# Kernel tuning notes

Measured on AMD Instinct MI355X. Metric: run time of the kernel, lower is better.

The kernel has to match this reference:

```python
import jax, jax.numpy as jnp
import numpy as np
from jax import lax

K = 5          # kernel_size
P = K // 2     # padding
DN = ('NCHW', 'OIHW', 'NCHW')


def _dwconv(z, wt, bt):
    # depthwise conv: z [b,c,h,w], wt [c,1,K,K], bt [c]
    c = z.shape[1]
    y = lax.conv_general_dilated(z, wt, (1, 1), [(P, P), (P, P)],
                                 feature_group_count=c, dimension_numbers=DN)
    return y + bt[None, :, None, None]


def setup_inputs() -> dict:
    key = jax.random.key(0)
    ks = jax.random.split(key, 8)
    b, c, h, w = 8, 64, 256, 256
    return {
        'x': jax.random.normal(ks[0], (b, c, h, w), jnp.float32),
        'w1': jax.random.normal(ks[1], (3, c, 1, K, K), jnp.float32) * 0.1,
        'b1': jax.random.normal(ks[2], (3, c), jnp.float32) * 0.1,
        'w2': jax.random.normal(ks[3], (3, c, 1, K, K), jnp.float32) * 0.1,
        'b2': jax.random.normal(ks[4], (3, c), jnp.float32) * 0.1,
        'wk': jax.random.normal(ks[5], (K * K * c, c), jnp.float32) * 0.1,
        'bk': jax.random.normal(ks[6], (K * K * c,), jnp.float32) * 0.1,
        'bias': jnp.zeros((c,), jnp.float32),
    }


def reference(x, w1, b1, w2, b2, wk, bk, bias):
    b, c, h, w = x.shape
    # avgpool 2x2 stride 2
    t = x.reshape(b, c, h // 2, 2, w // 2, 2).mean(axis=(3, 5))
    # Block1: 3 depthwise convs
    for i in range(3):
        t = _dwconv(t, w1[i], b1[i])
    # maxpool 2x2 stride 2
    hh, ww = t.shape[2], t.shape[3]
    t = t.reshape(b, c, hh // 2, 2, ww // 2, 2).max(axis=(3, 5))
    # Block2: 3 depthwise convs
    for i in range(3):
        t = _dwconv(t, w2[i], b2[i])
    # adaptive avg pool to 1x1 -> [b, c]
    g = t.mean(axis=(2, 3))
    # tokernel 1x1 conv -> per-sample depthwise kernels [b*c, 1, K, K]
    kern = (jnp.einsum('bc,oc->bo', g, wk) + bk).reshape(b * c, 1, K, K)
    # per-sample dynamic depthwise conv (groups = b*c)
    y = lax.conv_general_dilated(x.reshape(1, b * c, h, w), kern, (1, 1),
                                 [(P, P), (P, P)], feature_group_count=b * c,
                                 dimension_numbers=DN)
    return y.reshape(b, c, h, w) + bias[None, :, None, None]
```

## Files before the change

### kernel.cpp

```cpp
#include <hip/hip_runtime.h>

#define BB 8
#define CC 64
#define HH 256
#define WW 256
#define H1 128
#define W1 128
#define KK 5

template<int SS>
__device__ __forceinline__ void conv4x4(const float* __restrict__ src,
                                        const float* __restrict__ wr,
                                        float bv, float a[4][4])
{
#pragma unroll
    for (int i = 0; i < 4; i++)
#pragma unroll
        for (int j = 0; j < 4; j++) a[i][j] = bv;
#pragma unroll
    for (int ir = 0; ir < 8; ir++) {
        const float* s = src + ir * SS;
        float4 L = *(const float4*)s;
        float4 R = *(const float4*)(s + 4);
        float e[8] = {L.x, L.y, L.z, L.w, R.x, R.y, R.z, R.w};
#pragma unroll
        for (int i = 0; i < 4; i++) {
            const int ky = ir - i;
            if (ky >= 0 && ky < 5) {
#pragma unroll
                for (int kx = 0; kx < 5; kx++) {
                    const float wv = wr[ky * 5 + kx];
#pragma unroll
                    for (int j = 0; j < 4; j++) a[i][j] += e[j + kx] * wv;
                }
            }
        }
    }
}

template<int SS>
__device__ __forceinline__ void conv1x4(const float* __restrict__ src,
                                        const float* __restrict__ wr,
                                        float bv, float a[4])
{
#pragma unroll
    for (int j = 0; j < 4; j++) a[j] = bv;
#pragma unroll
    for (int ir = 0; ir < 5; ir++) {
        const float* s = src + ir * SS;
        float4 L = *(const float4*)s;
        float4 R = *(const float4*)(s + 4);
        float e[8] = {L.x, L.y, L.z, L.w, R.x, R.y, R.z, R.w};
#pragma unroll
        for (int kx = 0; kx < 5; kx++) {
            const float wv = wr[ir * 5 + kx];
#pragma unroll
            for (int j = 0; j < 4; j++) a[j] += e[j + kx] * wv;
        }
    }
}

__global__ __launch_bounds__(1024, 4) void k_block12(
    const float* __restrict__ x, const float* __restrict__ w1,
    const float* __restrict__ b1, const float* __restrict__ w2,
    const float* __restrict__ b2, float* __restrict__ g)
{
    const int plane = blockIdx.x;
    const int c = plane & 63;
    const int tid = threadIdx.x;

    __shared__ __align__(16) float sA[132 * 132];
    __shared__ __align__(16) float sB[132 * 132];
    __shared__ float red[16];

    const float* xp = x + (size_t)plane * HH * WW;

#pragma unroll
    for (int k = 0; k < 5; k++) {
        int i = tid + k * 1024;
        if (i < 132 * 132 / 4)
            ((float4*)sB)[i] = make_float4(0.f, 0.f, 0.f, 0.f);
    }

#pragma unroll
    for (int k = 0; k < 9; k++) {
        int i = tid + k * 1024;
        if (i < 132 * 66) {
            int r = i / 66, c2 = i % 66;
            float2 v = make_float2(0.f, 0.f);
            if (r >= 2 && r < 130 && c2 >= 1 && c2 <= 64) {
                int pr = r - 2;
                int xc = 4 * c2 - 4;
                float4 a0 = *(const float4*)(xp + (size_t)(2 * pr) * WW + xc);
                float4 a1 = *(const float4*)(xp + (size_t)(2 * pr + 1) * WW + xc);
                v.x = 0.25f * (a0.x + a0.y + a1.x + a1.y);
                v.y = 0.25f * (a0.z + a0.w + a1.z + a1.w);
            }
            *(float2*)&sA[r * 132 + 2 * c2] = v;
        }
    }
    __syncthreads();

    {
        const int tr = (tid >> 5) * 4, tc = (tid & 31) * 4;
#pragma unroll
        for (int cv = 0; cv < 3; cv++) {
            const float* src = (cv & 1) ? sB : sA;
            float* dst = (cv & 1) ? sA : sB;
            float wr[25];
#pragma unroll
            for (int k = 0; k < 25; k++) wr[k] = w1[cv * CC * 25 + c * 25 + k];
            const float bv = b1[cv * CC + c];
            float a[4][4];
            conv4x4<132>(&src[tr * 132 + tc], wr, bv, a);
#pragma unroll
            for (int i = 0; i < 4; i++) {
                float2* d = (float2*)&dst[(tr + i + 2) * 132 + tc + 2];
                d[0] = make_float2(a[i][0], a[i][1]);
                d[1] = make_float2(a[i][2], a[i][3]);
            }
            __syncthreads();
        }
    }

    float* pB = sA;
    float* pC = sA + 5440;
    for (int i = tid; i < 68 * 76; i += 1024) {
        int r = i / 76, cc2 = i % 76;
        float v = 0.f;
        if (r >= 2 && r < 66 && cc2 >= 2 && cc2 < 66) {
            const float* p = &sB[(size_t)(2 * (r - 2) + 2) * 132 + 2 * (cc2 - 2) + 2];
            v = fmaxf(fmaxf(p[0], p[1]), fmaxf(p[132], p[133]));
        }
        pB[i] = v;
        pC[i] = 0.f;
    }
    __syncthreads();

    const int r = tid >> 4, c0 = (tid & 15) * 4;
    {
        float wr[25];
#pragma unroll
        for (int k = 0; k < 25; k++) wr[k] = w2[0 * CC * 25 + c * 25 + k];
        float a[4];
        conv1x4<76>(&pB[r * 76 + c0], wr, b2[0 * CC + c], a);
        float2* d = (float2*)&pC[(r + 2) * 76 + c0 + 2];
        d[0] = make_float2(a[0], a[1]);
        d[1] = make_float2(a[2], a[3]);
    }
    __syncthreads();
    {
        float wr[25];
#pragma unroll
        for (int k = 0; k < 25; k++) wr[k] = w2[1 * CC * 25 + c * 25 + k];
        float a[4];
        conv1x4<76>(&pC[r * 76 + c0], wr, b2[1 * CC + c], a);
        float2* d = (float2*)&pB[(r + 2) * 76 + c0 + 2];
        d[0] = make_float2(a[0], a[1]);
        d[1] = make_float2(a[2], a[3]);
    }
    __syncthreads();
    float s;
    {
        float wr[25];
#pragma unroll
        for (int k = 0; k < 25; k++) wr[k] = w2[2 * CC * 25 + c * 25 + k];
        float a[4];
        conv1x4<76>(&pB[r * 76 + c0], wr, b2[2 * CC + c], a);
        s = a[0] + a[1] + a[2] + a[3];
    }
#pragma unroll
    for (int off = 32; off > 0; off >>= 1) s += __shfl_down(s, off);
    if ((tid & 63) == 0) red[tid >> 6] = s;
    __syncthreads();
    if (tid == 0) {
        float t = 0.f;
#pragma unroll
        for (int k = 0; k < 16; k++) t += red[k];
        g[plane] = t * (1.f / 4096.f);
    }
}

__global__ __launch_bounds__(256) void k_kern(
    const float* __restrict__ g, const float* __restrict__ wk,
    const float* __restrict__ bk, float* __restrict__ kern)
{
    const int o = blockIdx.x * 256 + threadIdx.x;
    const int b = o / 1600, oo = o - b * 1600;
    float v = bk[oo];
    const float* wp = wk + (size_t)oo * 64;
    const float* gp = g + b * 64;
#pragma unroll 16
    for (int k = 0; k < 64; k++) v += gp[k] * wp[k];
    kern[o] = v;
}

__global__ __launch_bounds__(256) void k_dyn(
    const float* __restrict__ x, const float* __restrict__ kern,
    const float* __restrict__ bias, float* __restrict__ out)
{
    const int plane = blockIdx.z;
    const int tx = blockIdx.x, ty = blockIdx.y;
    const int tid = threadIdx.x;

    __shared__ __align__(16) float sx[68 * 76];

    const float* xp = x + (size_t)plane * HH * WW;
    const int R0 = ty * 64, C0 = tx * 64;

#pragma unroll
    for (int k = 0; k < 5; k++) {
        int i = tid + k * 256;
        if (i < 68 * 18) {
            int r = i / 18, q = i - r * 18;
            int gr = R0 - 2 + r;
            int gc = C0 - 4 + 4 * q;
            float4 v = make_float4(0.f, 0.f, 0.f, 0.f);
            if ((unsigned)gr < HH && (unsigned)gc < WW)
                v = *(const float4*)(xp + (size_t)gr * WW + gc);
            *(float4*)&sx[r * 76 + 4 * q] = v;
        }
    }

    float w[25];
#pragma unroll
    for (int k = 0; k < 25; k++) w[k] = kern[(size_t)plane * 25 + k];
    const float bv = bias[plane & 63];

    __syncthreads();

    const int tr = (tid >> 4) * 4;
    const int tc = (tid & 15) * 4;
    float acc[4][4];
#pragma unroll
    for (int i = 0; i < 4; i++)
#pragma unroll
        for (int j = 0; j < 4; j++) acc[i][j] = bv;

#pragma unroll
    for (int ir = 0; ir < 8; ir++) {
        const float* s = &sx[(tr + ir) * 76 + tc];
        float4 A = *(const float4*)s;
        float4 B4 = *(const float4*)(s + 4);
        float4 Cv = *(const float4*)(s + 8);
        float e[12] = {A.x, A.y, A.z, A.w, B4.x, B4.y, B4.z, B4.w,
                       Cv.x, Cv.y, Cv.z, Cv.w};
#pragma unroll
        for (int i = 0; i < 4; i++) {
            const int ky = ir - i;
            if (ky >= 0 && ky < 5) {
#pragma unroll
                for (int kx = 0; kx < 5; kx++) {
                    const float wv = w[ky * 5 + kx];
#pragma unroll
                    for (int j = 0; j < 4; j++) acc[i][j] += e[j + kx + 2] * wv;
                }
            }
        }
    }

    float* op = out + (size_t)plane * HH * WW + (size_t)(R0 + tr) * WW + C0 + tc;
#pragma unroll
    for (int i = 0; i < 4; i++)
        *(float4*)(op + (size_t)i * WW) = make_float4(acc[i][0], acc[i][1], acc[i][2], acc[i][3]);
}

extern "C" void kernel_launch(void* const* d_in, const int* in_sizes, int n_in,
                              void* d_out, int out_size, void* d_ws, size_t ws_size,
                              hipStream_t stream)
{
    const float* x    = (const float*)d_in[0];
    const float* w1   = (const float*)d_in[1];
    const float* b1   = (const float*)d_in[2];
    const float* w2   = (const float*)d_in[3];
    const float* b2   = (const float*)d_in[4];
    const float* wk   = (const float*)d_in[5];
    const float* bk   = (const float*)d_in[6];
    const float* bias = (const float*)d_in[7];
    float* out = (float*)d_out;

    float* ws   = (float*)d_ws;
    float* g    = ws;
    float* kern = ws + 512;

    k_block12<<<dim3(512), 1024, 0, stream>>>(x, w1, b1, w2, b2, g);
    k_kern<<<dim3(50), 256, 0, stream>>>(g, wk, bk, kern);
    k_dyn<<<dim3(4, 4, 512), 256, 0, stream>>>(x, kern, bias, out);
}
```

Baseline: 121.4 us.

## Split fused block kernel into row-tiled block1 and separate block2 kernels

The single per-plane kernel, which used about 139KB of shared memory and 1024 threads, is replaced by k_a1. k_a1 processes half a plane per block (64 rows plus a 6-row halo, recomputed redundantly), and masks halo results to emulate zero padding between convs. It writes the maxpooled 64x64 map to workspace, and a new kernel k_b does the three block2 convs with 2x4 outputs per thread. The goal is more blocks, smaller shared memory and higher occupancy for the dominant early stage. The cost is halo recompute, an extra global round trip for the intermediate, and one more launch.

```diff
diff --git a/kernel.cpp b/kernel.cpp
--- a/kernel.cpp
+++ b/kernel.cpp
@@ -4,14 +4,12 @@
 #define CC 64
 #define HH 256
 #define WW 256
-#define H1 128
-#define W1 128
 #define KK 5
 
 template<int SS>
-__device__ __forceinline__ void conv4x4(const float* __restrict__ src,
-                                        const float* __restrict__ wr,
-                                        float bv, float a[4][4])
+__device__ __forceinline__ void conv4x4_e12(const float* __restrict__ src,
+                                            const float* __restrict__ wr,
+                                            float bv, float a[4][4])
 {
 #pragma unroll
     for (int i = 0; i < 4; i++)
@@ -20,9 +18,10 @@
 #pragma unroll
     for (int ir = 0; ir < 8; ir++) {
         const float* s = src + ir * SS;
-        float4 L = *(const float4*)s;
-        float4 R = *(const float4*)(s + 4);
-        float e[8] = {L.x, L.y, L.z, L.w, R.x, R.y, R.z, R.w};
+        float4 A = *(const float4*)s;
+        float4 B = *(const float4*)(s + 4);
+        float4 C = *(const float4*)(s + 8);
+        float e[12] = {A.x, A.y, A.z, A.w, B.x, B.y, B.z, B.w, C.x, C.y, C.z, C.w};
 #pragma unroll
         for (int i = 0; i < 4; i++) {
             const int ky = ir - i;
@@ -31,7 +30,7 @@
                 for (int kx = 0; kx < 5; kx++) {
                     const float wv = wr[ky * 5 + kx];
 #pragma unroll
-                    for (int j = 0; j < 4; j++) a[i][j] += e[j + kx] * wv;
+                    for (int j = 0; j < 4; j++) a[i][j] += e[2 + j + kx] * wv;
                 }
             }
         }
@@ -39,135 +38,194 @@
 }
 
 template<int SS>
-__device__ __forceinline__ void conv1x4(const float* __restrict__ src,
-                                        const float* __restrict__ wr,
-                                        float bv, float a[4])
-{
-#pragma unroll
-    for (int j = 0; j < 4; j++) a[j] = bv;
-#pragma unroll
-    for (int ir = 0; ir < 5; ir++) {
+__device__ __forceinline__ void conv2x4_e12(const float* __restrict__ src,
+                                            const float* __restrict__ wr,
+                                            float bv, float a[2][4])
+{
+#pragma unroll
+    for (int i = 0; i < 2; i++)
+#pragma unroll
+        for (int j = 0; j < 4; j++) a[i][j] = bv;
+#pragma unroll
+    for (int ir = 0; ir < 6; ir++) {
         const float* s = src + ir * SS;
-        float4 L = *(const float4*)s;
-        float4 R = *(const float4*)(s + 4);
-        float e[8] = {L.x, L.y, L.z, L.w, R.x, R.y, R.z, R.w};
-#pragma unroll
-        for (int kx = 0; kx < 5; kx++) {
-            const float wv = wr[ir * 5 + kx];
-#pragma unroll
-            for (int j = 0; j < 4; j++) a[j] += e[j + kx] * wv;
-        }
-    }
-}
-
-__global__ __launch_bounds__(1024, 4) void k_block12(
+        float4 A = *(const float4*)s;
+        float4 B = *(const float4*)(s + 4);
+        float4 C = *(const float4*)(s + 8);
+        float e[12] = {A.x, A.y, A.z, A.w, B.x, B.y, B.z, B.w, C.x, C.y, C.z, C.w};
+#pragma unroll
+        for (int i = 0; i < 2; i++) {
+            const int ky = ir - i;
+            if (ky >= 0 && ky < 5) {
+#pragma unroll
+                for (int kx = 0; kx < 5; kx++) {
+                    const float wv = wr[ky * 5 + kx];
+#pragma unroll
+                    for (int j = 0; j < 4; j++) a[i][j] += e[2 + j + kx] * wv;
+                }
+            }
+        }
+    }
+}
+
+__global__ __launch_bounds__(512, 6) void k_a1(
     const float* __restrict__ x, const float* __restrict__ w1,
-    const float* __restrict__ b1, const float* __restrict__ w2,
+    const float* __restrict__ b1, float* __restrict__ t2)
+{
+    const int plane = blockIdx.x;
+    const int c = plane & 63;
+    const int by = blockIdx.y;
+    const int R0 = by * 64;
+    const int tid = threadIdx.x;
+
+    __shared__ __align__(16) float sb[76 * 144];
+
+    const float* xp = x + (size_t)plane * HH * WW;
+
+#pragma unroll
+    for (int k = 0; k < 6; k++) {
+        int i = tid + k * 512;
+        if (i < 76 * 36) {
+            int r = i / 36, q = i % 36;
+            int pr = R0 - 6 + r;
+            float4 v = make_float4(0.f, 0.f, 0.f, 0.f);
+            if (q >= 2 && q <= 33 && (unsigned)pr < 128u) {
+                int xc = 8 * q - 16;
+                const float* p0 = xp + (size_t)(2 * pr) * WW + xc;
+                const float* p1 = p0 + WW;
+                float4 a0 = *(const float4*)p0;
+                float4 a1 = *(const float4*)(p0 + 4);
+                float4 b0 = *(const float4*)p1;
+                float4 b1v = *(const float4*)(p1 + 4);
+                v.x = 0.25f * (a0.x + a0.y + b0.x + b0.y);
+                v.y = 0.25f * (a0.z + a0.w + b0.z + b0.w);
+                v.z = 0.25f * (a1.x + a1.y + b1v.x + b1v.y);
+                v.w = 0.25f * (a1.z + a1.w + b1v.z + b1v.w);
+            }
+            *(float4*)&sb[r * 144 + 4 * q] = v;
+        }
+    }
+    __syncthreads();
+
+#pragma unroll
+    for (int cv = 0; cv < 3; cv++) {
+        float wr[25];
+#pragma unroll
+        for (int k = 0; k < 25; k++) wr[k] = w1[cv * CC * 25 + c * 25 + k];
+        const float bv = b1[cv * CC + c];
+
+        float a0[4][4], a1[4][4];
+        const int v0 = tid / 34, u0 = tid % 34;
+        conv4x4_e12<144>(&sb[(4 * v0) * 144 + 4 * u0], wr, bv, a0);
+        {
+            const bool cok = (u0 >= 1 && u0 <= 32);
+#pragma unroll
+            for (int i = 0; i < 4; i++) {
+                int gi = R0 - 4 + 4 * v0 + i;
+                bool ok = cok && ((unsigned)gi < 128u);
+#pragma unroll
+                for (int j = 0; j < 4; j++) if (!ok) a0[i][j] = 0.f;
+            }
+        }
+        const int t1i = tid + 512;
+        const bool has2 = t1i < 612;
+        const int v1 = t1i / 34, u1 = t1i % 34;
+        if (has2) {
+            conv4x4_e12<144>(&sb[(4 * v1) * 144 + 4 * u1], wr, bv, a1);
+            const bool cok = (u1 >= 1 && u1 <= 32);
+#pragma unroll
+            for (int i = 0; i < 4; i++) {
+                int gi = R0 - 4 + 4 * v1 + i;
+                bool ok = cok && ((unsigned)gi < 128u);
+#pragma unroll
+                for (int j = 0; j < 4; j++) if (!ok) a1[i][j] = 0.f;
+            }
+        }
+        __syncthreads();
+#pragma unroll
+        for (int i = 0; i < 4; i++)
+            *(float4*)&sb[(4 * v0 + 2 + i) * 144 + 4 * u0 + 4] =
+                make_float4(a0[i][0], a0[i][1], a0[i][2], a0[i][3]);
+        if (has2) {
+#pragma unroll
+            for (int i = 0; i < 4; i++)
+                *(float4*)&sb[(4 * v1 + 2 + i) * 144 + 4 * u1 + 4] =
+                    make_float4(a1[i][0], a1[i][1], a1[i][2], a1[i][3]);
+        }
+        __syncthreads();
+    }
+
+    {
+        const int mr = tid >> 4;
+        const int k2 = tid & 15;
+        const float* p0 = &sb[(6 + 2 * mr) * 144 + 8 + 8 * k2];
+        const float* p1 = p0 + 144;
+        float4 A = *(const float4*)p0;
+        float4 B = *(const float4*)(p0 + 4);
+        float4 C = *(const float4*)p1;
+        float4 D = *(const float4*)(p1 + 4);
+        float4 o;
+        o.x = fmaxf(fmaxf(A.x, A.y), fmaxf(C.x, C.y));
+        o.y = fmaxf(fmaxf(A.z, A.w), fmaxf(C.z, C.w));
+        o.z = fmaxf(fmaxf(B.x, B.y), fmaxf(D.x, D.y));
+        o.w = fmaxf(fmaxf(B.z, B.w), fmaxf(D.z, D.w));
+        *(float4*)&t2[((size_t)plane * 64 + by * 32 + mr) * 64 + 4 * k2] = o;
+    }
+}
+
+__global__ __launch_bounds__(512, 4) void k_b(
+    const float* __restrict__ t2, const float* __restrict__ w2,
     const float* __restrict__ b2, float* __restrict__ g)
 {
     const int plane = blockIdx.x;
     const int c = plane & 63;
     const int tid = threadIdx.x;
 
-    __shared__ __align__(16) float sA[132 * 132];
-    __shared__ __align__(16) float sB[132 * 132];
-    __shared__ float red[16];
-
-    const float* xp = x + (size_t)plane * HH * WW;
-
-#pragma unroll
-    for (int k = 0; k < 5; k++) {
-        int i = tid + k * 1024;
-        if (i < 132 * 132 / 4)
-            ((float4*)sB)[i] = make_float4(0.f, 0.f, 0.f, 0.f);
-    }
-
-#pragma unroll
-    for (int k = 0; k < 9; k++) {
-        int i = tid + k * 1024;
-        if (i < 132 * 66) {
-            int r = i / 66, c2 = i % 66;
-            float2 v = make_float2(0.f, 0.f);
-            if (r >= 2 && r < 130 && c2 >= 1 && c2 <= 64) {
-                int pr = r - 2;
-                int xc = 4 * c2 - 4;
-                float4 a0 = *(const float4*)(xp + (size_t)(2 * pr) * WW + xc);
-                float4 a1 = *(const float4*)(xp + (size_t)(2 * pr + 1) * WW + xc);
-                v.x = 0.25f * (a0.x + a0.y + a1.x + a1.y);
-                v.y = 0.25f * (a0.z + a0.w + a1.z + a1.w);
-            }
-            *(float2*)&sA[r * 132 + 2 * c2] = v;
+    __shared__ __align__(16) float sb[68 * 72];
+    __shared__ float red[8];
+
+    const float* tp = t2 + (size_t)plane * 4096;
+
+#pragma unroll
+    for (int k = 0; k < 3; k++) {
+        int i = tid + k * 512;
+        if (i < 68 * 18) {
+            int r = i / 18, q = i % 18;
+            float4 v = make_float4(0.f, 0.f, 0.f, 0.f);
+            if (r >= 2 && r < 66 && q >= 1 && q <= 16)
+                v = *(const float4*)(tp + (size_t)(r - 2) * 64 + 4 * (q - 1));
+            *(float4*)&sb[r * 72 + 4 * q] = v;
         }
     }
     __syncthreads();
 
-    {
-        const int tr = (tid >> 5) * 4, tc = (tid & 31) * 4;
-#pragma unroll
-        for (int cv = 0; cv < 3; cv++) {
-            const float* src = (cv & 1) ? sB : sA;
-            float* dst = (cv & 1) ? sA : sB;
-            float wr[25];
-#pragma unroll
-            for (int k = 0; k < 25; k++) wr[k] = w1[cv * CC * 25 + c * 25 + k];
-            const float bv = b1[cv * CC + c];
-            float a[4][4];
-            conv4x4<132>(&src[tr * 132 + tc], wr, bv, a);
-#pragma unroll
-            for (int i = 0; i < 4; i++) {
-                float2* d = (float2*)&dst[(tr + i + 2) * 132 + tc + 2];
-                d[0] = make_float2(a[i][0], a[i][1]);
-                d[1] = make_float2(a[i][2], a[i][3]);
-            }
-            __syncthreads();
-        }
-    }
-
-    float* pB = sA;
-    float* pC = sA + 5440;
-    for (int i = tid; i < 68 * 76; i += 1024) {
-        int r = i / 76, cc2 = i % 76;
-        float v = 0.f;
-        if (r >= 2 && r < 66 && cc2 >= 2 && cc2 < 66) {
-            const float* p = &sB[(size_t)(2 * (r - 2) + 2) * 132 + 2 * (cc2 - 2) + 2];
-            v = fmaxf(fmaxf(p[0], p[1]), fmaxf(p[132], p[133]));
-        }
-        pB[i] = v;
-        pC[i] = 0.f;
-    }
-    __syncthreads();
-
-    const int r = tid >> 4, c0 = (tid & 15) * 4;
-    {
+    const int v = tid >> 4, u = tid & 15;
+    const float* rb = &sb[(2 * v) * 72 + 4 * u];
+    float* wb = &sb[(2 * v + 2) * 72 + 4 * u + 4];
+
+#pragma unroll
+    for (int cv = 0; cv < 2; cv++) {
         float wr[25];
 #pragma unroll
-        for (int k = 0; k < 25; k++) wr[k] = w2[0 * CC * 25 + c * 25 + k];
-        float a[4];
-        conv1x4<76>(&pB[r * 76 + c0], wr, b2[0 * CC + c], a);
-        float2* d = (float2*)&pC[(r + 2) * 76 + c0 + 2];
-        d[0] = make_float2(a[0], a[1]);
-        d[1] = make_float2(a[2], a[3]);
-    }
-    __syncthreads();
-    {
-        float wr[25];
-#pragma unroll
-        for (int k = 0; k < 25; k++) wr[k] = w2[1 * CC * 25 + c * 25 + k];
-        float a[4];
-        conv1x4<76>(&pC[r * 76 + c0], wr, b2[1 * CC + c], a);
-        float2* d = (float2*)&pB[(r + 2) * 76 + c0 + 2];
-        d[0] = make_float2(a[0], a[1]);
-        d[1] = make_float2(a[2], a[3]);
-    }
-    __syncthreads();
+        for (int k = 0; k < 25; k++) wr[k] = w2[cv * CC * 25 + c * 25 + k];
+        float a[2][4];
+        conv2x4_e12<72>(rb, wr, b2[cv * CC + c], a);
+        __syncthreads();
+#pragma unroll
+        for (int i = 0; i < 2; i++)
+            *(float4*)(wb + i * 72) = make_float4(a[i][0], a[i][1], a[i][2], a[i][3]);
+        __syncthreads();
+    }
+
     float s;
     {
         float wr[25];
 #pragma unroll
         for (int k = 0; k < 25; k++) wr[k] = w2[2 * CC * 25 + c * 25 + k];
-        float a[4];
-        conv1x4<76>(&pB[r * 76 + c0], wr, b2[2 * CC + c], a);
-        s = a[0] + a[1] + a[2] + a[3];
+        float a[2][4];
+        conv2x4_e12<72>(rb, wr, b2[2 * CC + c], a);
+        s = (a[0][0] + a[0][1] + a[0][2] + a[0][3]) +
+            (a[1][0] + a[1][1] + a[1][2] + a[1][3]);
     }
 #pragma unroll
     for (int off = 32; off > 0; off >>= 1) s += __shfl_down(s, off);
@@ -176,7 +234,7 @@
     if (tid == 0) {
         float t = 0.f;
 #pragma unroll
-        for (int k = 0; k < 16; k++) t += red[k];
+        for (int k = 0; k < 8; k++) t += red[k];
         g[plane] = t * (1.f / 4096.f);
     }
 }
@@ -280,10 +338,12 @@
     float* out = (float*)d_out;
 
     float* ws   = (float*)d_ws;
-    float* g    = ws;
-    float* kern = ws + 512;
-
-    k_block12<<<dim3(512), 1024, 0, stream>>>(x, w1, b1, w2, b2, g);
+    float* t2   = ws;
+    float* g    = ws + 2097152;
+    float* kern = g + 512;
+
+    k_a1<<<dim3(512, 2), 512, 0, stream>>>(x, w1, b1, t2);
+    k_b<<<dim3(512), 512, 0, stream>>>(t2, w2, b2, g);
     k_kern<<<dim3(50), 256, 0, stream>>>(g, wk, bk, kern);
     k_dyn<<<dim3(4, 4, 512), 256, 0, stream>>>(x, kern, bias, out);
 }
```

New measurement: 264.0 us. 2.17x slower.
